# Optimization experiments

Measured on AMD Instinct MI355X. Metric: run time of the kernel, lower is better.

Reference implementation:

```python
import jax, jax.numpy as jnp
import numpy as np

B, NV, FD = 16, 128, 8192
T_TEMP = 0.2      # self.T
MARGIN = 1.0      # nn.TripletMarginLoss default
EPS = 1e-6        # pairwise_distance eps


def _l2norm(x):
    # torch F.normalize(dim=1): x / max(||x||, 1e-12)
    nrm = jnp.maximum(jnp.linalg.norm(x, axis=-1, keepdims=True), 1e-12)
    return x / nrm


def _ssl_parts(qb, kb, nb, num_gt):
    # qb,kb,nb: [NV, FD] flattened reid embeddings for one image
    qv = _l2norm(qb)[:num_gt]          # [g, FD]
    kv = _l2norm(kb)[:num_gt]          # [g, FD]
    nv = _l2norm(nb)                   # [NV, FD] (negatives are NOT sliced)
    g = num_gt
    S = qv @ kv.T                      # [g, g] all pairwise dots (replaces torch.dot loops)
    # similarity-matrix loss
    sm = jnp.sum((S - jnp.eye(g, dtype=S.dtype)) ** 2) / (g * g)
    # pairwise distances with torch eps convention: ||a - b + eps||_2
    # = sqrt(||a||^2 + ||b||^2 - 2 a.b + 2*eps*(sum(a)-sum(b)) + D*eps^2); ||a||=||b||=1
    sq = qv.sum(axis=1)                # [g]
    sk = kv.sum(axis=1)                # [g]
    const = FD * EPS * EPS
    d_qk = jnp.sqrt(jnp.maximum(2.0 - 2.0 * S + 2.0 * EPS * (sq[:, None] - sk[None, :]) + const, 0.0))
    d_kq = jnp.sqrt(jnp.maximum(2.0 - 2.0 * S.T + 2.0 * EPS * (sk[:, None] - sq[None, :]) + const, 0.0))
    off = 1.0 - jnp.eye(g, dtype=S.dtype)
    # triplet: anc=q_i,pos=k_i,neg=k_j  and  anc=k_i,pos=q_i,neg=q_j, j != i
    tri1 = jnp.sum(jax.nn.relu(jnp.diag(d_qk)[:, None] - d_qk + MARGIN) * off)
    tri2 = jnp.sum(jax.nn.relu(jnp.diag(d_kq)[:, None] - d_kq + MARGIN) * off)
    tri_sum = tri1 + tri2
    # cycle consistency: |q_i.k_j - k_i.q_j| = |S[i,j] - S[j,i]|
    cyc = jnp.sum(jnp.abs(S - S.T) * off) / (g * (g - 1))
    # InfoNCE: l_pos = q_i.k_i, l_neg = q @ n.T
    l_pos = jnp.diag(S)[:, None]       # [g, 1]
    l_neg = qv @ nv.T                  # [g, NV]
    logits = jnp.concatenate([l_pos, l_neg], axis=1) / T_TEMP
    ce = jnp.mean(jax.nn.logsumexp(logits, axis=1) - logits[:, 0])  # CE with labels=0
    return sm, tri_sum, cyc, ce / g


def setup_inputs() -> dict:
    key = jax.random.key(0)
    kq, kk, kn = jax.random.split(key, 3)
    q = jax.random.normal(kq, (B, NV, FD), dtype=jnp.float32)
    k = jax.random.normal(kk, (B, NV, FD), dtype=jnp.float32)
    n = jax.random.normal(kn, (B, NV, FD), dtype=jnp.float32)
    return {"q": q, "k": k, "n": n, "num_gt": NV}


def reference(q, k, n, num_gt):
    sm, tri, cyc, ce = jax.vmap(lambda a, b, c: _ssl_parts(a, b, c, num_gt))(q, k, n)
    tri_cnt = 2 * num_gt * (num_gt - 1)
    # original bug: tri_loss accumulates across batches while tri_cnt resets,
    # so each batch contributes cumsum(tri)[b] / tri_cnt
    ssl = jnp.sum(sm) + jnp.sum(jnp.cumsum(tri)) / tri_cnt + jnp.sum(cyc) + jnp.sum(ce)
    return ssl
```

## Files before the change

### kernel.cpp

```cpp
#include <hip/hip_runtime.h>
#include <cstdint>
#include <cstddef>

#define B_N   16
#define G_N   128
#define FD_N  8192
#define KSPLIT 16
#define KC    512
#define BK    64
#define NSTAGE 8

typedef unsigned short u16;
typedef u16  u16x8 __attribute__((ext_vector_type(8)));
typedef __bf16 bf16x8 __attribute__((ext_vector_type(8)));
typedef float f32x16 __attribute__((ext_vector_type(16)));

#define QSUM_P   0
#define QSSQ_P   32768
#define KSUM_P   65536
#define KSSQ_P   98304
#define NSSQ_P   131072
#define PART_OFF_F 430080

__device__ __forceinline__ u16 f2bf(float f) {
    uint32_t u = __float_as_uint(f);
    u += 0x7FFFu + ((u >> 16) & 1u);
    return (u16)(u >> 16);
}

#define LGKM0_BAR() do { asm volatile("s_waitcnt lgkmcnt(0)" ::: "memory"); \
                         __builtin_amdgcn_s_barrier(); } while (0)

__global__ __launch_bounds__(512, 2)
void k_gemm(const float* __restrict__ q, const float* __restrict__ kM,
            const float* __restrict__ nM, float* __restrict__ ws,
            float* __restrict__ out)
{
    __shared__ __align__(16) u16 smem[2 * 24576];

    const int tid = threadIdx.x;
    const int blk = blockIdx.x;
    const int b   = blk >> 4;
    const int kch = blk & 15;

    if (blk == 0 && tid == 0) out[0] = 0.f;

    const int lane  = tid & 63;
    const int wv    = tid >> 6;
    const int wm    = wv >> 2;
    const int wn    = wv & 3;
    const int khalf = lane >> 5;
    const int lrow  = lane & 31;
    const int g     = lane >> 4;
    const int cc    = lane & 15;

    const size_t mat_off = (size_t)b * (G_N * FD_N) + (size_t)kch * KC;
    const float* Ap = q + mat_off;
    const float* Bw = (wv < 4 ? kM : nM) + mat_off;

    float4 La[4], Lb[8];
    float sA_[4] = {0,0,0,0}, qA_[4] = {0,0,0,0};
    float sB_[8] = {0,0,0,0,0,0,0,0}, qB_[8] = {0,0,0,0,0,0,0,0};

    f32x16 acc[2][2];
    #pragma unroll
    for (int m = 0; m < 2; ++m)
      #pragma unroll
      for (int n = 0; n < 2; ++n)
        #pragma unroll
        for (int e = 0; e < 16; ++e) acc[m][n][e] = 0.f;

#define ISSUE(S) do {                                                          \
        const size_t ko_ = (size_t)((S)*BK + cc*4);                            \
        _Pragma("unroll")                                                      \
        for (int i = 0; i < 4; ++i)                                            \
            La[i] = *(const float4*)(Ap + (size_t)(wv*16 + i*4 + g)*FD_N + ko_); \
        _Pragma("unroll")                                                      \
        for (int i = 0; i < 8; ++i)                                            \
            Lb[i] = *(const float4*)(Bw + (size_t)(wn*32 + i*4 + g)*FD_N + ko_); \
    } while (0)

#define CVTWRITE(BUF) do {                                                     \
        u16* dA_ = smem + (BUF)*24576;                                         \
        u16* dB_ = dA_ + 8192;                                                 \
        _Pragma("unroll")                                                      \
        for (int i = 0; i < 4; ++i) {                                          \
            const int r_ = wv*16 + i*4 + g;                                    \
            float4 v = La[i];                                                  \
            sA_[i] += (v.x + v.y) + (v.z + v.w);                               \
            qA_[i] += v.x*v.x + v.y*v.y + v.z*v.z + v.w*v.w;                   \
            uint2 p;                                                           \
            p.x = (uint32_t)f2bf(v.x) | ((uint32_t)f2bf(v.y) << 16);           \
            p.y = (uint32_t)f2bf(v.z) | ((uint32_t)f2bf(v.w) << 16);           \
            *(uint2*)(dA_ + r_*64 + ((cc ^ ((r_&7)<<1)) << 2)) = p;            \
        }                                                                      \
        _Pragma("unroll")                                                      \
        for (int i = 0; i < 8; ++i) {                                          \
            const int r_  = wn*32 + i*4 + g;                                   \
            const int rl_ = r_ + (wv < 4 ? 0 : 128);                           \
            float4 v = Lb[i];                                                  \
            sB_[i] += (v.x + v.y) + (v.z + v.w);                               \
            qB_[i] += v.x*v.x + v.y*v.y + v.z*v.z + v.w*v.w;                   \
            uint2 p;                                                           \
            p.x = (uint32_t)f2bf(v.x) | ((uint32_t)f2bf(v.y) << 16);           \
            p.y = (uint32_t)f2bf(v.z) | ((uint32_t)f2bf(v.w) << 16);           \
            *(uint2*)(dB_ + rl_*64 + ((cc ^ ((rl_&7)<<1)) << 2)) = p;          \
        }                                                                      \
    } while (0)

#define FRAG(DP, R, KCH)                                                       \
    __builtin_bit_cast(bf16x8, *(const u16x8*)((DP) + (R)*64 +                 \
        ((((KCH)*2 + khalf) ^ ((R)&7)) << 3)))

#define COMPUTE(BUF) do {                                                      \
        const u16* dA_ = smem + (BUF)*24576;                                   \
        const u16* dB_ = dA_ + 8192;                                           \
        __builtin_amdgcn_s_setprio(1);                                         \
        _Pragma("unroll")                                                      \
        for (int kc = 0; kc < 4; ++kc) {                                       \
            bf16x8 a0_ = FRAG(dA_, wm*64 +      lrow, kc);                     \
            bf16x8 a1_ = FRAG(dA_, wm*64 + 32 + lrow, kc);                     \
            bf16x8 b0_ = FRAG(dB_, wn*64 +      lrow, kc);                     \
            bf16x8 b1_ = FRAG(dB_, wn*64 + 32 + lrow, kc);                     \
            acc[0][0] = __builtin_amdgcn_mfma_f32_32x32x16_bf16(a0_, b0_, acc[0][0], 0,0,0); \
            acc[0][1] = __builtin_amdgcn_mfma_f32_32x32x16_bf16(a0_, b1_, acc[0][1], 0,0,0); \
            acc[1][0] = __builtin_amdgcn_mfma_f32_32x32x16_bf16(a1_, b0_, acc[1][0], 0,0,0); \
            acc[1][1] = __builtin_amdgcn_mfma_f32_32x32x16_bf16(a1_, b1_, acc[1][1], 0,0,0); \
        }                                                                      \
        __builtin_amdgcn_s_setprio(0);                                         \
    } while (0)

    ISSUE(0);
    CVTWRITE(0);
    LGKM0_BAR();

    for (int s = 0; s < NSTAGE; ++s) {
        if (s + 1 < NSTAGE) ISSUE(s + 1);
        COMPUTE(s & 1);
        if (s + 1 < NSTAGE) {
            LGKM0_BAR();
            CVTWRITE((s + 1) & 1);
            LGKM0_BAR();
        }
    }

    u16* part = (u16*)(ws + PART_OFF_F);
    #pragma unroll
    for (int m = 0; m < 2; ++m)
      #pragma unroll
      for (int n = 0; n < 2; ++n) {
        const int colg = wn*64 + n*32 + lrow;
        const int ho   = colg >> 7;
        const int col  = colg & 127;
        u16* pb = part + (size_t)(b*2 + ho) * 262144;
        const int rbase = wm*64 + m*32 + 4*khalf;
        #pragma unroll
        for (int reg = 0; reg < 16; ++reg) {
            const int row = rbase + (reg & 3) + 8*(reg >> 2);
            pb[(row*16 + kch)*128 + col] = f2bf(acc[m][n][reg]);
        }
      }

    #pragma unroll
    for (int i = 0; i < 4; ++i)
        #pragma unroll
        for (int msk = 8; msk >= 1; msk >>= 1) {
            sA_[i] += __shfl_xor(sA_[i], msk, 64);
            qA_[i] += __shfl_xor(qA_[i], msk, 64);
        }
    #pragma unroll
    for (int i = 0; i < 8; ++i)
        #pragma unroll
        for (int msk = 8; msk >= 1; msk >>= 1) {
            sB_[i] += __shfl_xor(sB_[i], msk, 64);
            qB_[i] += __shfl_xor(qB_[i], msk, 64);
        }
    if (cc == 0) {
        #pragma unroll
        for (int i = 0; i < 4; ++i) {
            const int o = kch*2048 + b*G_N + (wv*16 + i*4 + g);
            ws[QSUM_P + o] = sA_[i]; ws[QSSQ_P + o] = qA_[i];
        }
        #pragma unroll
        for (int i = 0; i < 8; ++i) {
            const int o = kch*2048 + b*G_N + (wn*32 + i*4 + g);
            if (wv < 4) { ws[KSUM_P + o] = sB_[i]; ws[KSSQ_P + o] = qB_[i]; }
            else        { ws[NSSQ_P + o] = qB_[i]; }
        }
    }
#undef ISSUE
#undef CVTWRITE
#undef FRAG
#undef COMPUTE
}

__global__ __launch_bounds__(1024)
void k_fin(float* __restrict__ ws, float* __restrict__ out)
{
    __shared__ float S_lds[G_N * G_N];
    __shared__ float invq[128], nrk[128], nrn[128], sqv[128], skv[128];
    __shared__ float ddq[128], ddk[128], smrow[128], cerow[128];
    __shared__ float wred[16];

    const int b = blockIdx.x;
    const int t = threadIdx.x;
    const float c0 = (float)FD_N * 1e-6f * 1e-6f;

    if (t < 128) {
        float qs=0.f, qq=0.f, ks=0.f, kq=0.f, nq=0.f;
        #pragma unroll
        for (int kc = 0; kc < KSPLIT; ++kc) {
            const int o = kc*2048 + b*G_N + t;
            qs += ws[QSUM_P + o]; qq += ws[QSSQ_P + o];
            ks += ws[KSUM_P + o]; kq += ws[KSSQ_P + o];
            nq += ws[NSSQ_P + o];
        }
        const float iq = 1.f / fmaxf(sqrtf(qq), 1e-12f);
        const float ik = 1.f / fmaxf(sqrtf(kq), 1e-12f);
        invq[t] = iq; nrk[t] = ik;
        nrn[t]  = 1.f / fmaxf(sqrtf(nq), 1e-12f);
        sqv[t]  = qs * iq; skv[t] = ks * ik;
    }
    __syncthreads();

    const int i  = t >> 3;
    const int c8 = t & 7;
    const int j0 = c8 * 16;
    const u16* part = (const u16*)(ws + PART_OFF_F);
    const float iqv = invq[i];

    {
        float s[16];
        #pragma unroll
        for (int e = 0; e < 16; ++e) s[e] = 0.f;
        const u16* p0 = part + (size_t)(b*2) * 262144 + i*2048 + j0;
        #pragma unroll
        for (int kc = 0; kc < KSPLIT; ++kc) {
            const u16x8 h0 = *(const u16x8*)(p0 + kc*128);
            const u16x8 h1 = *(const u16x8*)(p0 + kc*128 + 8);
            #pragma unroll
            for (int e = 0; e < 8; ++e) {
                s[e]   += __uint_as_float(((uint32_t)h0[e]) << 16);
                s[e+8] += __uint_as_float(((uint32_t)h1[e]) << 16);
            }
        }
        float sm = 0.f;
        #pragma unroll
        for (int e = 0; e < 16; ++e) {
            const int j = j0 + e;
            const float Sv = s[e] * iqv * nrk[j];
            S_lds[i*G_N + j] = Sv;
            const float d = Sv - (j == i ? 1.f : 0.f);
            sm += d*d;
        }
        #pragma unroll
        for (int m = 4; m >= 1; m >>= 1) sm += __shfl_xor(sm, m, 64);
        if (c8 == 0) smrow[i] = sm;
    }
    {
        float s[16];
        #pragma unroll
        for (int e = 0; e < 16; ++e) s[e] = 0.f;
        const u16* p1 = part + (size_t)(b*2 + 1) * 262144 + i*2048 + j0;
        #pragma unroll
        for (int kc = 0; kc < KSPLIT; ++kc) {
            const u16x8 h0 = *(const u16x8*)(p1 + kc*128);
            const u16x8 h1 = *(const u16x8*)(p1 + kc*128 + 8);
            #pragma unroll
            for (int e = 0; e < 8; ++e) {
                s[e]   += __uint_as_float(((uint32_t)h0[e]) << 16);
                s[e+8] += __uint_as_float(((uint32_t)h1[e]) << 16);
            }
        }
        float ea = 0.f;
        #pragma unroll
        for (int e = 0; e < 16; ++e)
            ea += __expf(5.f * s[e] * iqv * nrn[j0 + e]);
        #pragma unroll
        for (int m = 4; m >= 1; m >>= 1) ea += __shfl_xor(ea, m, 64);
        if (c8 == 0) cerow[i] = ea;
    }
    __syncthreads();

    if (t < 128) {
        const float Stt = S_lds[t*G_N + t];
        ddq[t] = sqrtf(fmaxf(2.f - 2.f*Stt + 2e-6f*(sqv[t] - skv[t]) + c0, 0.f));
        ddk[t] = sqrtf(fmaxf(2.f - 2.f*Stt + 2e-6f*(skv[t] - sqv[t]) + c0, 0.f));
    }
    __syncthreads();

    float tri = 0.f, cyc = 0.f, rowterm = 0.f;
    #pragma unroll
    for (int p2 = 0; p2 < 16; ++p2) {
        const int idx = p2*1024 + t;
        const int ii = idx >> 7, jj = idx & 127;
        if (ii != jj) {
            const float S_ij = S_lds[ii*G_N + jj];
            const float dqk = sqrtf(fmaxf(2.f - 2.f*S_ij + 2e-6f*(sqv[ii]-skv[jj]) + c0, 0.f));
            tri += fmaxf(ddq[ii] - dqk + 1.f, 0.f);
            const float dkq = sqrtf(fmaxf(2.f - 2.f*S_ij + 2e-6f*(skv[jj]-sqv[ii]) + c0, 0.f));
            tri += fmaxf(ddk[jj] - dkq + 1.f, 0.f);
            cyc += fabsf(S_ij - S_lds[jj*G_N + ii]);
        }
    }
    if (t < 128) {
        const float lp = 5.f * S_lds[t*G_N + t];
        const float ce = __logf(cerow[t] + __expf(lp)) - lp;
        rowterm = smrow[t] * (1.f/16384.f) + ce * (1.f/16384.f);
    }
    float contrib = rowterm + cyc * (1.f/16256.f)
                  + (float)(B_N - b) * tri * (1.f/32512.f);
    #pragma unroll
    for (int m = 32; m >= 1; m >>= 1) contrib += __shfl_xor(contrib, m, 64);
    if ((t & 63) == 0) wred[t >> 6] = contrib;
    __syncthreads();
    if (t == 0) {
        float tot = 0.f;
        #pragma unroll
        for (int w = 0; w < 16; ++w) tot += wred[w];
        atomicAdd(out, tot);
    }
}

extern "C" void kernel_launch(void* const* d_in, const int* in_sizes, int n_in,
                              void* d_out, int out_size, void* d_ws, size_t ws_size,
                              hipStream_t stream)
{
    const float* q  = (const float*)d_in[0];
    const float* kM = (const float*)d_in[1];
    const float* nM = (const float*)d_in[2];
    float* ws  = (float*)d_ws;
    float* out = (float*)d_out;

    k_gemm<<<B_N * KSPLIT, 512, 0, stream>>>(q, kM, nM, ws, out);
    k_fin<<<B_N, 1024, 0, stream>>>(ws, out);
}
```

Baseline: 230.5 us.

## Split finalize kernel across row blocks to raise parallelism

The finalize kernel now runs 128 blocks of 512 threads, one block per 16-row slice of each batch, instead of 16 blocks of 1024 threads. Each block rebuilds only its own rows of S plus the column slice it needs for the cycle term, and reduces the diagonal directly from the partial buffers. This spreads the split-K reduction and the loss math over many more compute units, at the cost of redundant per-row norm reductions in every block and re-reading partials for the columns and diagonal.

```diff
diff --git a/kernel.cpp b/kernel.cpp
--- a/kernel.cpp
+++ b/kernel.cpp
@@ -11,6 +11,7 @@
 #define NSTAGE 8
 
 typedef unsigned short u16;
+typedef u16  u16x4 __attribute__((ext_vector_type(4)));
 typedef u16  u16x8 __attribute__((ext_vector_type(8)));
 typedef __bf16 bf16x8 __attribute__((ext_vector_type(8)));
 typedef float f32x16 __attribute__((ext_vector_type(16)));
@@ -26,6 +27,9 @@
     uint32_t u = __float_as_uint(f);
     u += 0x7FFFu + ((u >> 16) & 1u);
     return (u16)(u >> 16);
+}
+__device__ __forceinline__ float bf2f(u16 h) {
+    return __uint_as_float(((uint32_t)h) << 16);
 }
 
 #define LGKM0_BAR() do { asm volatile("s_waitcnt lgkmcnt(0)" ::: "memory"); \
@@ -194,122 +198,157 @@
 #undef COMPUTE
 }
 
-__global__ __launch_bounds__(1024)
-void k_fin(float* __restrict__ ws, float* __restrict__ out)
+__global__ __launch_bounds__(512)
+void k_fin2(float* __restrict__ ws, float* __restrict__ out)
 {
-    __shared__ float S_lds[G_N * G_N];
-    __shared__ float invq[128], nrk[128], nrn[128], sqv[128], skv[128];
-    __shared__ float ddq[128], ddk[128], smrow[128], cerow[128];
-    __shared__ float wred[16];
-
-    const int b = blockIdx.x;
-    const int t = threadIdx.x;
+    __shared__ float invq[128], nrk[128], nrn[128], sqv[128], skv[128], diagv[128], ddk[128];
+    __shared__ float Sown[16][128];
+    __shared__ float Scol[128][17];
+    __shared__ float smrow[16], cerow[16], ddqv[16], cev[16];
+    __shared__ float wred[8];
+
+    const int blk = blockIdx.x;
+    const int b   = blk >> 3;
+    const int i0  = (blk & 7) * 16;
+    const int t   = threadIdx.x;
     const float c0 = (float)FD_N * 1e-6f * 1e-6f;
-
-    if (t < 128) {
+    const u16* pb0 = (const u16*)(ws + PART_OFF_F) + (size_t)(b*2) * 262144;
+    const u16* pb1 = pb0 + 262144;
+
+    {
+        const int r = t >> 2, p = t & 3;
         float qs=0.f, qq=0.f, ks=0.f, kq=0.f, nq=0.f;
         #pragma unroll
-        for (int kc = 0; kc < KSPLIT; ++kc) {
-            const int o = kc*2048 + b*G_N + t;
+        for (int e = 0; e < 4; ++e) {
+            const int o = (p*4 + e)*2048 + b*G_N + r;
             qs += ws[QSUM_P + o]; qq += ws[QSSQ_P + o];
             ks += ws[KSUM_P + o]; kq += ws[KSSQ_P + o];
             nq += ws[NSSQ_P + o];
         }
-        const float iq = 1.f / fmaxf(sqrtf(qq), 1e-12f);
-        const float ik = 1.f / fmaxf(sqrtf(kq), 1e-12f);
-        invq[t] = iq; nrk[t] = ik;
-        nrn[t]  = 1.f / fmaxf(sqrtf(nq), 1e-12f);
-        sqv[t]  = qs * iq; skv[t] = ks * ik;
+        #pragma unroll
+        for (int m = 1; m <= 2; m <<= 1) {
+            qs += __shfl_xor(qs, m, 64); qq += __shfl_xor(qq, m, 64);
+            ks += __shfl_xor(ks, m, 64); kq += __shfl_xor(kq, m, 64);
+            nq += __shfl_xor(nq, m, 64);
+        }
+        if (p == 0) {
+            const float iq = 1.f / fmaxf(sqrtf(qq), 1e-12f);
+            const float ik = 1.f / fmaxf(sqrtf(kq), 1e-12f);
+            invq[r] = iq; nrk[r] = ik;
+            nrn[r]  = 1.f / fmaxf(sqrtf(nq), 1e-12f);
+            sqv[r]  = qs * iq; skv[r] = ks * ik;
+        }
     }
     __syncthreads();
 
-    const int i  = t >> 3;
-    const int c8 = t & 7;
-    const int j0 = c8 * 16;
-    const u16* part = (const u16*)(ws + PART_OFF_F);
+    const int il  = t >> 5;
+    const int ct  = t & 31;
+    const int i   = i0 + il;
+    const int c0i = ct * 4;
     const float iqv = invq[i];
 
     {
-        float s[16];
-        #pragma unroll
-        for (int e = 0; e < 16; ++e) s[e] = 0.f;
-        const u16* p0 = part + (size_t)(b*2) * 262144 + i*2048 + j0;
-        #pragma unroll
-        for (int kc = 0; kc < KSPLIT; ++kc) {
-            const u16x8 h0 = *(const u16x8*)(p0 + kc*128);
-            const u16x8 h1 = *(const u16x8*)(p0 + kc*128 + 8);
+        float s0=0.f, s1=0.f, s2=0.f, s3=0.f;
+        const u16* p = pb0 + (size_t)(i*16)*128 + c0i;
+        #pragma unroll
+        for (int kc = 0; kc < 16; ++kc) {
+            const u16x4 h = *(const u16x4*)(p + kc*128);
+            s0 += bf2f(h[0]); s1 += bf2f(h[1]); s2 += bf2f(h[2]); s3 += bf2f(h[3]);
+        }
+        float4 Sv;
+        Sv.x = s0 * iqv * nrk[c0i];     Sv.y = s1 * iqv * nrk[c0i+1];
+        Sv.z = s2 * iqv * nrk[c0i+2];   Sv.w = s3 * iqv * nrk[c0i+3];
+        *(float4*)&Sown[il][c0i] = Sv;
+        float sm = 0.f;
+        {
+            float d = Sv.x - (c0i   == i ? 1.f : 0.f); sm += d*d;
+            d = Sv.y - (c0i+1 == i ? 1.f : 0.f); sm += d*d;
+            d = Sv.z - (c0i+2 == i ? 1.f : 0.f); sm += d*d;
+            d = Sv.w - (c0i+3 == i ? 1.f : 0.f); sm += d*d;
+        }
+        #pragma unroll
+        for (int m = 16; m >= 1; m >>= 1) sm += __shfl_xor(sm, m, 64);
+        if (ct == 0) smrow[il] = sm;
+    }
+    {
+        float s0=0.f, s1=0.f, s2=0.f, s3=0.f;
+        const u16* p = pb1 + (size_t)(i*16)*128 + c0i;
+        #pragma unroll
+        for (int kc = 0; kc < 16; ++kc) {
+            const u16x4 h = *(const u16x4*)(p + kc*128);
+            s0 += bf2f(h[0]); s1 += bf2f(h[1]); s2 += bf2f(h[2]); s3 += bf2f(h[3]);
+        }
+        float ea = __expf(5.f * s0 * iqv * nrn[c0i])
+                 + __expf(5.f * s1 * iqv * nrn[c0i+1])
+                 + __expf(5.f * s2 * iqv * nrn[c0i+2])
+                 + __expf(5.f * s3 * iqv * nrn[c0i+3]);
+        #pragma unroll
+        for (int m = 16; m >= 1; m >>= 1) ea += __shfl_xor(ea, m, 64);
+        if (ct == 0) cerow[il] = ea;
+    }
+
+    {
+        const int j = t >> 2, p = t & 3;
+        float cs[16];
+        #pragma unroll
+        for (int e = 0; e < 16; ++e) cs[e] = 0.f;
+        float dg = 0.f;
+        #pragma unroll
+        for (int e2 = 0; e2 < 4; ++e2) {
+            const int kc = p*4 + e2;
+            const u16* pp = pb0 + (size_t)(j*16 + kc)*128;
+            const u16x8 h0 = *(const u16x8*)(pp + i0);
+            const u16x8 h1 = *(const u16x8*)(pp + i0 + 8);
             #pragma unroll
             for (int e = 0; e < 8; ++e) {
-                s[e]   += __uint_as_float(((uint32_t)h0[e]) << 16);
-                s[e+8] += __uint_as_float(((uint32_t)h1[e]) << 16);
+                cs[e]   += bf2f(h0[e]);
+                cs[e+8] += bf2f(h1[e]);
             }
-        }
-        float sm = 0.f;
-        #pragma unroll
-        for (int e = 0; e < 16; ++e) {
-            const int j = j0 + e;
-            const float Sv = s[e] * iqv * nrk[j];
-            S_lds[i*G_N + j] = Sv;
-            const float d = Sv - (j == i ? 1.f : 0.f);
-            sm += d*d;
-        }
-        #pragma unroll
-        for (int m = 4; m >= 1; m >>= 1) sm += __shfl_xor(sm, m, 64);
-        if (c8 == 0) smrow[i] = sm;
-    }
-    {
-        float s[16];
-        #pragma unroll
-        for (int e = 0; e < 16; ++e) s[e] = 0.f;
-        const u16* p1 = part + (size_t)(b*2 + 1) * 262144 + i*2048 + j0;
-        #pragma unroll
-        for (int kc = 0; kc < KSPLIT; ++kc) {
-            const u16x8 h0 = *(const u16x8*)(p1 + kc*128);
-            const u16x8 h1 = *(const u16x8*)(p1 + kc*128 + 8);
+            dg += bf2f(pp[j]);
+        }
+        #pragma unroll
+        for (int m = 1; m <= 2; m <<= 1) {
             #pragma unroll
-            for (int e = 0; e < 8; ++e) {
-                s[e]   += __uint_as_float(((uint32_t)h0[e]) << 16);
-                s[e+8] += __uint_as_float(((uint32_t)h1[e]) << 16);
-            }
-        }
-        float ea = 0.f;
-        #pragma unroll
-        for (int e = 0; e < 16; ++e)
-            ea += __expf(5.f * s[e] * iqv * nrn[j0 + e]);
-        #pragma unroll
-        for (int m = 4; m >= 1; m >>= 1) ea += __shfl_xor(ea, m, 64);
-        if (c8 == 0) cerow[i] = ea;
+            for (int e = 0; e < 16; ++e) cs[e] += __shfl_xor(cs[e], m, 64);
+            dg += __shfl_xor(dg, m, 64);
+        }
+        if (p == 0) {
+            const float sj = invq[j];
+            #pragma unroll
+            for (int e = 0; e < 16; ++e)
+                Scol[j][e] = cs[e] * sj * nrk[i0 + e];
+            diagv[j] = dg * sj * nrk[j];
+        }
     }
     __syncthreads();
 
     if (t < 128) {
-        const float Stt = S_lds[t*G_N + t];
-        ddq[t] = sqrtf(fmaxf(2.f - 2.f*Stt + 2e-6f*(sqv[t] - skv[t]) + c0, 0.f));
-        ddk[t] = sqrtf(fmaxf(2.f - 2.f*Stt + 2e-6f*(skv[t] - sqv[t]) + c0, 0.f));
+        ddk[t] = sqrtf(fmaxf(2.f - 2.f*diagv[t] + 2e-6f*(skv[t] - sqv[t]) + c0, 0.f));
+    } else if (t < 144) {
+        const int r = i0 + (t - 128);
+        ddqv[t-128] = sqrtf(fmaxf(2.f - 2.f*diagv[r] + 2e-6f*(sqv[r] - skv[r]) + c0, 0.f));
+    } else if (t < 160) {
+        const int r  = i0 + (t - 144);
+        const float lp = 5.f * diagv[r];
+        cev[t-144] = __logf(cerow[t-144] + __expf(lp)) - lp;
     }
     __syncthreads();
 
-    float tri = 0.f, cyc = 0.f, rowterm = 0.f;
-    #pragma unroll
-    for (int p2 = 0; p2 < 16; ++p2) {
-        const int idx = p2*1024 + t;
-        const int ii = idx >> 7, jj = idx & 127;
-        if (ii != jj) {
-            const float S_ij = S_lds[ii*G_N + jj];
-            const float dqk = sqrtf(fmaxf(2.f - 2.f*S_ij + 2e-6f*(sqv[ii]-skv[jj]) + c0, 0.f));
-            tri += fmaxf(ddq[ii] - dqk + 1.f, 0.f);
-            const float dkq = sqrtf(fmaxf(2.f - 2.f*S_ij + 2e-6f*(skv[jj]-sqv[ii]) + c0, 0.f));
-            tri += fmaxf(ddk[jj] - dkq + 1.f, 0.f);
-            cyc += fabsf(S_ij - S_lds[jj*G_N + ii]);
-        }
-    }
-    if (t < 128) {
-        const float lp = 5.f * S_lds[t*G_N + t];
-        const float ce = __logf(cerow[t] + __expf(lp)) - lp;
-        rowterm = smrow[t] * (1.f/16384.f) + ce * (1.f/16384.f);
-    }
-    float contrib = rowterm + cyc * (1.f/16256.f)
-                  + (float)(B_N - b) * tri * (1.f/32512.f);
+    float tri = 0.f, cyc = 0.f;
+    #pragma unroll
+    for (int e = 0; e < 4; ++e) {
+        const int j = c0i + e;
+        if (j != i) {
+            const float Sij = Sown[il][j];
+            const float dqk = sqrtf(fmaxf(2.f - 2.f*Sij + 2e-6f*(sqv[i] - skv[j]) + c0, 0.f));
+            tri += fmaxf(ddqv[il] - dqk + 1.f, 0.f);
+            const float dkq = sqrtf(fmaxf(2.f - 2.f*Sij + 2e-6f*(skv[j] - sqv[i]) + c0, 0.f));
+            tri += fmaxf(ddk[j] - dkq + 1.f, 0.f);
+            cyc += fabsf(Sij - Scol[j][il]);
+        }
+    }
+    float contrib = cyc * (1.f/16256.f) + (float)(B_N - b) * tri * (1.f/32512.f);
+    if (t < 16) contrib += (smrow[t] + cev[t]) * (1.f/16384.f);
     #pragma unroll
     for (int m = 32; m >= 1; m >>= 1) contrib += __shfl_xor(contrib, m, 64);
     if ((t & 63) == 0) wred[t >> 6] = contrib;
@@ -317,7 +356,7 @@
     if (t == 0) {
         float tot = 0.f;
         #pragma unroll
-        for (int w = 0; w < 16; ++w) tot += wred[w];
+        for (int w = 0; w < 8; ++w) tot += wred[w];
         atomicAdd(out, tot);
     }
 }
@@ -333,5 +372,5 @@
     float* out = (float*)d_out;
 
     k_gemm<<<B_N * KSPLIT, 512, 0, stream>>>(q, kM, nM, ws, out);
-    k_fin<<<B_N, 1024, 0, stream>>>(ws, out);
-}
+    k_fin2<<<B_N * 8, 512, 0, stream>>>(ws, out);
+}
```

Result: faster. 221.6 us (-3.9%).
